# Optimization experiments

Hardware: AMD Instinct MI355X
Metric: run time of the kernel (lower is better)

Reference implementation:

```python
import jax, jax.numpy as jnp
import numpy as np

N = 100000   # nodes
E = 1000000  # edges
D = 64       # in = out = edge_dim
G = 16       # graphs


def setup_inputs() -> dict:
    key = jax.random.key(0)
    ks = jax.random.split(key, 12)
    s = 1.0 / np.sqrt(D)
    inp = {
        "x": jax.random.normal(ks[0], (N, D), dtype=jnp.float32),
        "edge_index": jax.random.randint(ks[1], (2, E), 0, N, dtype=jnp.int64),
        "edge_attr": jax.random.normal(ks[2], (E, D), dtype=jnp.float32),
        "u": jax.random.normal(ks[3], (G, D), dtype=jnp.float32),
        "batch": jax.random.randint(ks[4], (N,), 0, G, dtype=jnp.int64),
        # ResGatedGraphConv params (lin_key, lin_query, lin_value, lin_edge, lin_skip)
        "Wk": jax.random.uniform(ks[5], (D, D), jnp.float32, -s, s),
        "bk": jnp.zeros((D,), jnp.float32),
        "Wq": jax.random.uniform(ks[6], (D, D), jnp.float32, -s, s),
        "bq": jnp.zeros((D,), jnp.float32),
        "Wv": jax.random.uniform(ks[7], (D, D), jnp.float32, -s, s),
        "bv": jnp.zeros((D,), jnp.float32),
        "We": jax.random.uniform(ks[8], (D, D), jnp.float32, -s, s),
        "be": jnp.zeros((D,), jnp.float32),
        "Ws": jax.random.uniform(ks[9], (D, D), jnp.float32, -s, s),
        "bs": jnp.zeros((D,), jnp.float32),
    }
    return inp


def reference(x, edge_index, edge_attr, u, batch,
              Wk, bk, Wq, bq, Wv, bv, We, be, Ws, bs):
    src, dst = edge_index[0], edge_index[1]  # j -> i (aggregate at dst)
    # node-level projections (done once, then gathered per edge)
    k = x @ Wk.T + bk
    q = x @ Wq.T + bq
    v = x @ Wv.T + bv
    e = edge_attr @ We.T + be            # [E, D]
    k_i = k[dst] + e
    q_j = q[src] + e
    v_j = v[src] + e
    msg = jax.nn.sigmoid(k_i + q_j) * v_j  # gated message [E, D]
    agg = jax.ops.segment_sum(msg, dst, num_segments=N)
    out = jax.nn.relu(agg + x @ Ws.T + bs)
    return (out, edge_attr, u, edge_index)
```

## Files before the change

kernel.cpp:

```cpp
#include <hip/hip_runtime.h>

#define NN 100000
#define NE 1000000

#define OUT_EA  6400000ull
#define OUT_U   70400000ull
#define OUT_EI  70401024ull

typedef short bf16x8 __attribute__((ext_vector_type(8)));
typedef float f32x16 __attribute__((ext_vector_type(16)));

#define Z16 {0.f,0.f,0.f,0.f,0.f,0.f,0.f,0.f,0.f,0.f,0.f,0.f,0.f,0.f,0.f,0.f}

#define MFMA(a, b, c) __builtin_amdgcn_mfma_f32_32x32x16_bf16((a), (b), (c), 0, 0, 0)

__device__ __forceinline__ short f2bf(float f) {
    unsigned u = __float_as_uint(f);
    u += 0x7fff + ((u >> 16) & 1);
    return (short)(u >> 16);
}
__device__ __forceinline__ bf16x8 pack8(float4 a, float4 b) {
    bf16x8 r;
    r[0] = f2bf(a.x); r[1] = f2bf(a.y); r[2] = f2bf(a.z); r[3] = f2bf(a.w);
    r[4] = f2bf(b.x); r[5] = f2bf(b.y); r[6] = f2bf(b.z); r[7] = f2bf(b.w);
    return r;
}

__device__ __forceinline__ void load_bfrags(const float* __restrict__ W, int lane,
                                            bf16x8 bf[4][2]) {
    const float4* w4 = (const float4*)W;
    const int ln = lane & 31, kh = lane >> 5;
#pragma unroll
    for (int c = 0; c < 4; c++)
#pragma unroll
        for (int h = 0; h < 2; h++) {
            const float4* p = w4 + (h * 32 + ln) * 16 + c * 4 + kh * 2;
            bf[c][h] = pack8(p[0], p[1]);
        }
}

__global__ __launch_bounds__(256, 4) void proj_kernel(
    const float* __restrict__ x,
    const float* __restrict__ Wk, const float* __restrict__ bk,
    const float* __restrict__ Wq, const float* __restrict__ bq,
    const float* __restrict__ Wv, const float* __restrict__ bv,
    float* __restrict__ ko, float* __restrict__ qo, float* __restrict__ vo,
    float* __restrict__ agg)
{
    const int tid = threadIdx.x;

    if (blockIdx.y == 3) {
        const float4 z = make_float4(0.f, 0.f, 0.f, 0.f);
        for (int i = blockIdx.x * 256 + tid; i < 1600000; i += 200192)
            ((float4*)agg)[i] = z;
        return;
    }

    const int lane = tid & 63, wave = tid >> 6;
    const int ln = lane & 31, kh = lane >> 5;

    const int rbase = blockIdx.x * 128 + wave * 32;
    if (rbase >= NN) return;

    const float* W = blockIdx.y == 0 ? Wk : blockIdx.y == 1 ? Wq : Wv;
    const float* b = blockIdx.y == 0 ? bk : blockIdx.y == 1 ? bq : bv;
    float*       o = blockIdx.y == 0 ? ko : blockIdx.y == 1 ? qo : vo;

    bf16x8 bf[4][2];
    load_bfrags(W, lane, bf);
    const float bias0 = b[ln], bias1 = b[32 + ln];

    f32x16 acc0 = Z16, acc1 = Z16;
    const float4* a4 = (const float4*)x + (size_t)(rbase + ln) * 16 + kh * 2;
#pragma unroll
    for (int c = 0; c < 4; c++) {
        bf16x8 af = pack8(a4[c * 4], a4[c * 4 + 1]);
        acc0 = MFMA(af, bf[c][0], acc0);
        acc1 = MFMA(af, bf[c][1], acc1);
    }

#pragma unroll
    for (int r = 0; r < 16; r++) {
        int row = rbase + (r & 3) + 8 * (r >> 2) + 4 * kh;
        o[(size_t)row * 64 + ln]      = acc0[r] + bias0;
        o[(size_t)row * 64 + 32 + ln] = acc1[r] + bias1;
    }
}

__global__ __launch_bounds__(256, 3) void edge_kernel(
    const float* __restrict__ ea, const int* __restrict__ ei,
    const float* __restrict__ We, const float* __restrict__ be,
    const float* __restrict__ ko, const float* __restrict__ qo, const float* __restrict__ vo,
    float* __restrict__ agg, float* __restrict__ out)
{
    __shared__ int idx_lds[4][2][32];
    const int tid = threadIdx.x;
    const int lane = tid & 63, wave = tid >> 6;
    const int ln = lane & 31, kh = lane >> 5;

    bf16x8 bf[4][2];
    load_bfrags(We, lane, bf);
    const float be0 = be[ln], be1 = be[32 + ln];
    float* echo = out + OUT_EA;

    for (int gb = blockIdx.x * 128 + wave * 32; gb < NE; gb += gridDim.x * 128) {
        idx_lds[wave][kh][ln] = ei[kh * NE + gb + ln];

        const float4* a4 = (const float4*)ea + (size_t)(gb + ln) * 16 + kh * 2;
        float4*       e4 = (float4*)echo    + (size_t)(gb + ln) * 16 + kh * 2;

        f32x16 acc0 = Z16, acc1 = Z16;
#pragma unroll
        for (int c = 0; c < 4; c++) {
            float4 f0 = a4[c * 4], f1 = a4[c * 4 + 1];
            e4[c * 4] = f0; e4[c * 4 + 1] = f1;
            bf16x8 af = pack8(f0, f1);
            acc0 = MFMA(af, bf[c][0], acc0);
            acc1 = MFMA(af, bf[c][1], acc1);
        }

#pragma unroll
        for (int r = 0; r < 16; r++) {
            int row = (r & 3) + 8 * (r >> 2) + 4 * kh;
            int s = idx_lds[wave][0][row];
            int t = idx_lds[wave][1][row];
            int tb = t * 64, sb = s * 64;
            float ev0 = acc0[r] + be0, ev1 = acc1[r] + be1;
            float kd0 = ko[tb + ln],      kd1 = ko[tb + 32 + ln];
            float qj0 = qo[sb + ln],      qj1 = qo[sb + 32 + ln];
            float vj0 = vo[sb + ln],      vj1 = vo[sb + 32 + ln];
            float z0 = kd0 + qj0 + ev0 + ev0;
            float z1 = kd1 + qj1 + ev1 + ev1;
            float g0 = 1.0f / (1.0f + __expf(-z0));
            float g1 = 1.0f / (1.0f + __expf(-z1));
            atomicAdd(&agg[tb + ln],      g0 * (vj0 + ev0));
            atomicAdd(&agg[tb + 32 + ln], g1 * (vj1 + ev1));
        }
    }
}

__global__ __launch_bounds__(256, 4) void final_kernel(
    const float* __restrict__ x, const float* __restrict__ Ws, const float* __restrict__ bs,
    const float* __restrict__ agg, const float* __restrict__ u,
    const int* __restrict__ ei, float* __restrict__ out)
{
    const int tid = threadIdx.x;
    const int lane = tid & 63, wave = tid >> 6;
    const int ln = lane & 31, kh = lane >> 5;

    {
        int gtid = blockIdx.x * 256 + tid;
        if (gtid < 1024) out[OUT_U + gtid] = u[gtid];
        for (int i = gtid; i < 2000000; i += 200192)
            out[OUT_EI + i] = (float)ei[i];
    }

    const int rbase = blockIdx.x * 128 + wave * 32;
    if (rbase >= NN) return;

    bf16x8 bf[4][2];
    load_bfrags(Ws, lane, bf);
    const float bias0 = bs[ln], bias1 = bs[32 + ln];

    f32x16 acc0 = Z16, acc1 = Z16;
    const float4* a4 = (const float4*)x + (size_t)(rbase + ln) * 16 + kh * 2;
#pragma unroll
    for (int c = 0; c < 4; c++) {
        bf16x8 af = pack8(a4[c * 4], a4[c * 4 + 1]);
        acc0 = MFMA(af, bf[c][0], acc0);
        acc1 = MFMA(af, bf[c][1], acc1);
    }

#pragma unroll
    for (int r = 0; r < 16; r++) {
        int row = rbase + (r & 3) + 8 * (r >> 2) + 4 * kh;
        float r0 = acc0[r] + bias0 + agg[(size_t)row * 64 + ln];
        float r1 = acc1[r] + bias1 + agg[(size_t)row * 64 + 32 + ln];
        out[(size_t)row * 64 + ln]      = r0 > 0.0f ? r0 : 0.0f;
        out[(size_t)row * 64 + 32 + ln] = r1 > 0.0f ? r1 : 0.0f;
    }
}

extern "C" void kernel_launch(void* const* d_in, const int* in_sizes, int n_in,
                              void* d_out, int out_size, void* d_ws, size_t ws_size,
                              hipStream_t stream)
{
    const float* x  = (const float*)d_in[0];
    const int*   ei = (const int*)d_in[1];
    const float* ea = (const float*)d_in[2];
    const float* u  = (const float*)d_in[3];
    const float* Wk = (const float*)d_in[5];
    const float* bk = (const float*)d_in[6];
    const float* Wq = (const float*)d_in[7];
    const float* bq = (const float*)d_in[8];
    const float* Wv = (const float*)d_in[9];
    const float* bv = (const float*)d_in[10];
    const float* We = (const float*)d_in[11];
    const float* be = (const float*)d_in[12];
    const float* Ws = (const float*)d_in[13];
    const float* bs = (const float*)d_in[14];
    float* out = (float*)d_out;

    float* ws  = (float*)d_ws;
    float* ko  = ws;
    float* qo  = ws + 6400000;
    float* vo  = ws + 12800000;
    float* agg = ws + 19200000;

    proj_kernel <<<dim3(782, 4), 256, 0, stream>>>(x, Wk, bk, Wq, bq, Wv, bv, ko, qo, vo, agg);
    edge_kernel <<<2048, 256, 0, stream>>>(ea, ei, We, be, ko, qo, vo, agg, out);
    final_kernel<<<782, 256, 0, stream>>>(x, Ws, bs, agg, u, ei, out);
}
```

Before: 700.6 us.

## Store node projections in bf16, pack q/v, and batch gathers in edge kernel

The projection kernel now computes k, q and v in a single pass per block and writes k as bf16 and q/v as packed bf16 pairs in one 32-bit word. This halves the bytes gathered per edge and merges the q and v gathers into one load. The edge loop issues eight rows of gathers ahead of the math so more loads are in flight. In exchange, k, q and v lose precision through bf16 rounding, and the proj kernel uses more registers, so its occupancy bound is lowered.

After: 660.1 us. 5.8% less time.

```diff
diff --git a/kernel.cpp b/kernel.cpp
--- a/kernel.cpp
+++ b/kernel.cpp
@@ -14,15 +14,18 @@
 
 #define MFMA(a, b, c) __builtin_amdgcn_mfma_f32_32x32x16_bf16((a), (b), (c), 0, 0, 0)
 
-__device__ __forceinline__ short f2bf(float f) {
+__device__ __forceinline__ unsigned f2bf(float f) {
     unsigned u = __float_as_uint(f);
     u += 0x7fff + ((u >> 16) & 1);
-    return (short)(u >> 16);
+    return u >> 16;
+}
+__device__ __forceinline__ float bf2f(unsigned lo16) {
+    return __uint_as_float(lo16 << 16);
 }
 __device__ __forceinline__ bf16x8 pack8(float4 a, float4 b) {
     bf16x8 r;
-    r[0] = f2bf(a.x); r[1] = f2bf(a.y); r[2] = f2bf(a.z); r[3] = f2bf(a.w);
-    r[4] = f2bf(b.x); r[5] = f2bf(b.y); r[6] = f2bf(b.z); r[7] = f2bf(b.w);
+    r[0] = (short)f2bf(a.x); r[1] = (short)f2bf(a.y); r[2] = (short)f2bf(a.z); r[3] = (short)f2bf(a.w);
+    r[4] = (short)f2bf(b.x); r[5] = (short)f2bf(b.y); r[6] = (short)f2bf(b.z); r[7] = (short)f2bf(b.w);
     return r;
 }
 
@@ -39,17 +42,17 @@
         }
 }
 
-__global__ __launch_bounds__(256, 4) void proj_kernel(
+__global__ __launch_bounds__(256, 2) void proj_kernel(
     const float* __restrict__ x,
     const float* __restrict__ Wk, const float* __restrict__ bk,
     const float* __restrict__ Wq, const float* __restrict__ bq,
     const float* __restrict__ Wv, const float* __restrict__ bv,
-    float* __restrict__ ko, float* __restrict__ qo, float* __restrict__ vo,
+    unsigned short* __restrict__ k16, unsigned* __restrict__ qv,
     float* __restrict__ agg)
 {
     const int tid = threadIdx.x;
 
-    if (blockIdx.y == 3) {
+    if (blockIdx.y == 1) {
         const float4 z = make_float4(0.f, 0.f, 0.f, 0.f);
         for (int i = blockIdx.x * 256 + tid; i < 1600000; i += 200192)
             ((float4*)agg)[i] = z;
@@ -62,35 +65,38 @@
     const int rbase = blockIdx.x * 128 + wave * 32;
     if (rbase >= NN) return;
 
-    const float* W = blockIdx.y == 0 ? Wk : blockIdx.y == 1 ? Wq : Wv;
-    const float* b = blockIdx.y == 0 ? bk : blockIdx.y == 1 ? bq : bv;
-    float*       o = blockIdx.y == 0 ? ko : blockIdx.y == 1 ? qo : vo;
-
-    bf16x8 bf[4][2];
-    load_bfrags(W, lane, bf);
-    const float bias0 = b[ln], bias1 = b[32 + ln];
-
-    f32x16 acc0 = Z16, acc1 = Z16;
+    bf16x8 bk_[4][2], bq_[4][2], bv_[4][2];
+    load_bfrags(Wk, lane, bk_);
+    load_bfrags(Wq, lane, bq_);
+    load_bfrags(Wv, lane, bv_);
+    const float k0 = bk[ln], k1 = bk[32 + ln];
+    const float q0 = bq[ln], q1 = bq[32 + ln];
+    const float v0 = bv[ln], v1 = bv[32 + ln];
+
+    f32x16 ak0 = Z16, ak1 = Z16, aq0 = Z16, aq1 = Z16, av0 = Z16, av1 = Z16;
     const float4* a4 = (const float4*)x + (size_t)(rbase + ln) * 16 + kh * 2;
 #pragma unroll
     for (int c = 0; c < 4; c++) {
         bf16x8 af = pack8(a4[c * 4], a4[c * 4 + 1]);
-        acc0 = MFMA(af, bf[c][0], acc0);
-        acc1 = MFMA(af, bf[c][1], acc1);
+        ak0 = MFMA(af, bk_[c][0], ak0); ak1 = MFMA(af, bk_[c][1], ak1);
+        aq0 = MFMA(af, bq_[c][0], aq0); aq1 = MFMA(af, bq_[c][1], aq1);
+        av0 = MFMA(af, bv_[c][0], av0); av1 = MFMA(af, bv_[c][1], av1);
     }
 
 #pragma unroll
     for (int r = 0; r < 16; r++) {
-        int row = rbase + (r & 3) + 8 * (r >> 2) + 4 * kh;
-        o[(size_t)row * 64 + ln]      = acc0[r] + bias0;
-        o[(size_t)row * 64 + 32 + ln] = acc1[r] + bias1;
+        size_t row = rbase + (r & 3) + 8 * (r >> 2) + 4 * kh;
+        k16[row * 64 + ln]      = (unsigned short)f2bf(ak0[r] + k0);
+        k16[row * 64 + 32 + ln] = (unsigned short)f2bf(ak1[r] + k1);
+        qv[row * 64 + ln]      = f2bf(aq0[r] + q0) | (f2bf(av0[r] + v0) << 16);
+        qv[row * 64 + 32 + ln] = f2bf(aq1[r] + q1) | (f2bf(av1[r] + v1) << 16);
     }
 }
 
 __global__ __launch_bounds__(256, 3) void edge_kernel(
     const float* __restrict__ ea, const int* __restrict__ ei,
     const float* __restrict__ We, const float* __restrict__ be,
-    const float* __restrict__ ko, const float* __restrict__ qo, const float* __restrict__ vo,
+    const unsigned short* __restrict__ k16, const unsigned* __restrict__ qv,
     float* __restrict__ agg, float* __restrict__ out)
 {
     __shared__ int idx_lds[4][2][32];
@@ -120,21 +126,36 @@
         }
 
 #pragma unroll
-        for (int r = 0; r < 16; r++) {
-            int row = (r & 3) + 8 * (r >> 2) + 4 * kh;
-            int s = idx_lds[wave][0][row];
-            int t = idx_lds[wave][1][row];
-            int tb = t * 64, sb = s * 64;
-            float ev0 = acc0[r] + be0, ev1 = acc1[r] + be1;
-            float kd0 = ko[tb + ln],      kd1 = ko[tb + 32 + ln];
-            float qj0 = qo[sb + ln],      qj1 = qo[sb + 32 + ln];
-            float vj0 = vo[sb + ln],      vj1 = vo[sb + 32 + ln];
-            float z0 = kd0 + qj0 + ev0 + ev0;
-            float z1 = kd1 + qj1 + ev1 + ev1;
-            float g0 = 1.0f / (1.0f + __expf(-z0));
-            float g1 = 1.0f / (1.0f + __expf(-z1));
-            atomicAdd(&agg[tb + ln],      g0 * (vj0 + ev0));
-            atomicAdd(&agg[tb + 32 + ln], g1 * (vj1 + ev1));
+        for (int h = 0; h < 2; h++) {
+            int tb[8];
+            unsigned kr0[8], kr1[8], s0[8], s1[8];
+#pragma unroll
+            for (int i = 0; i < 8; i++) {
+                int r = h * 8 + i;
+                int row = (r & 3) + 8 * (r >> 2) + 4 * kh;
+                int s = idx_lds[wave][0][row];
+                int t = idx_lds[wave][1][row];
+                tb[i] = t * 64;
+                int sb = s * 64;
+                kr0[i] = k16[tb[i] + ln];
+                kr1[i] = k16[tb[i] + 32 + ln];
+                s0[i] = qv[sb + ln];
+                s1[i] = qv[sb + 32 + ln];
+            }
+#pragma unroll
+            for (int i = 0; i < 8; i++) {
+                int r = h * 8 + i;
+                float ev0 = acc0[r] + be0, ev1 = acc1[r] + be1;
+                float kd0 = bf2f(kr0[i]),        kd1 = bf2f(kr1[i]);
+                float qj0 = bf2f(s0[i] & 0xffffu), vj0 = __uint_as_float(s0[i] & 0xffff0000u);
+                float qj1 = bf2f(s1[i] & 0xffffu), vj1 = __uint_as_float(s1[i] & 0xffff0000u);
+                float z0 = kd0 + qj0 + ev0 + ev0;
+                float z1 = kd1 + qj1 + ev1 + ev1;
+                float g0 = 1.0f / (1.0f + __expf(-z0));
+                float g1 = 1.0f / (1.0f + __expf(-z1));
+                atomicAdd(&agg[tb[i] + ln],      g0 * (vj0 + ev0));
+                atomicAdd(&agg[tb[i] + 32 + ln], g1 * (vj1 + ev1));
+            }
         }
     }
 }
@@ -173,11 +194,11 @@
 
 #pragma unroll
     for (int r = 0; r < 16; r++) {
-        int row = rbase + (r & 3) + 8 * (r >> 2) + 4 * kh;
-        float r0 = acc0[r] + bias0 + agg[(size_t)row * 64 + ln];
-        float r1 = acc1[r] + bias1 + agg[(size_t)row * 64 + 32 + ln];
-        out[(size_t)row * 64 + ln]      = r0 > 0.0f ? r0 : 0.0f;
-        out[(size_t)row * 64 + 32 + ln] = r1 > 0.0f ? r1 : 0.0f;
+        size_t row = rbase + (r & 3) + 8 * (r >> 2) + 4 * kh;
+        float r0 = acc0[r] + bias0 + agg[row * 64 + ln];
+        float r1 = acc1[r] + bias1 + agg[row * 64 + 32 + ln];
+        out[row * 64 + ln]      = r0 > 0.0f ? r0 : 0.0f;
+        out[row * 64 + 32 + ln] = r1 > 0.0f ? r1 : 0.0f;
     }
 }
 
@@ -201,13 +222,12 @@
     const float* bs = (const float*)d_in[14];
     float* out = (float*)d_out;
 
-    float* ws  = (float*)d_ws;
-    float* ko  = ws;
-    float* qo  = ws + 6400000;
-    float* vo  = ws + 12800000;
-    float* agg = ws + 19200000;
-
-    proj_kernel <<<dim3(782, 4), 256, 0, stream>>>(x, Wk, bk, Wq, bq, Wv, bv, ko, qo, vo, agg);
-    edge_kernel <<<2048, 256, 0, stream>>>(ea, ei, We, be, ko, qo, vo, agg, out);
+    float* ws = (float*)d_ws;
+    unsigned short* k16 = (unsigned short*)ws;
+    unsigned*       qvp = (unsigned*)(ws + 3200000);
+    float*          agg = ws + 9600000;
+
+    proj_kernel <<<dim3(782, 2), 256, 0, stream>>>(x, Wk, bk, Wq, bq, Wv, bv, k16, qvp, agg);
+    edge_kernel <<<2048, 256, 0, stream>>>(ea, ei, We, be, k16, qvp, agg, out);
     final_kernel<<<782, 256, 0, stream>>>(x, Ws, bs, agg, u, ei, out);
 }
```
